# Kernel optimization log

Measured on AMD Instinct MI355X. Metric: run time of the kernel, lower is better.

Reference implementation:

```python
import jax, jax.numpy as jnp
import numpy as np

B, S, DIN, D, H = 32, 2048, 1024, 512, 8
NC, NM = 19, 10


def _mha(q_in, kv, Wq, bq, Wk, bk, Wv, bv, Wo, bo, add_mask):
    # q_in: [B,S,D]; kv: [K,D] (shared across batch); add_mask: [B,S,K] additive logit bias
    Bq, Sq, Dm = q_in.shape
    dh = Dm // H
    q = (q_in @ Wq + bq).reshape(Bq, Sq, H, dh)
    k = (kv @ Wk + bk).reshape(-1, H, dh)
    v = (kv @ Wv + bv).reshape(-1, H, dh)
    logits = jnp.einsum('bshd,khd->bhsk', q, k) / jnp.sqrt(jnp.float32(dh))
    attn = jax.nn.softmax(logits + add_mask[:, None, :, :], axis=-1)  # [B,H,S,K]
    out = jnp.einsum('bhsk,khd->bshd', attn, v).reshape(Bq, Sq, Dm)
    return out @ Wo + bo


def setup_inputs() -> dict:
    key = jax.random.key(0)
    ks = jax.random.split(key, 32)
    s = 0.02
    p = lambda i, shape: jax.random.normal(ks[i], shape, jnp.float32) * s
    z = lambda: jnp.zeros((D,), jnp.float32)
    return {
        'embeddings': jax.random.normal(ks[0], (B, S, DIN), jnp.float32),
        'embeddings_mask': jax.random.randint(ks[1], (B, S), 0, 2, jnp.int32),
        'post_mask': jax.random.randint(ks[2], (B, S), 0, 2, jnp.int32),
        'frame_mask': jax.random.randint(ks[3], (B, S), 0, 2, jnp.int32),
        'cultural_mask': jax.random.randint(ks[4], (B, NC), 0, 2, jnp.int32),
        'moral_mask': jax.random.randint(ks[5], (B, NM), 0, 2, jnp.int32),
        'W_lin': p(6, (DIN, D)), 'b_lin': z(),
        'cultural_table': p(7, (NC, D)), 'moral_table': p(8, (NM, D)),
        'c_Wq': p(9, (D, D)), 'c_bq': z(), 'c_Wk': p(10, (D, D)), 'c_bk': z(),
        'c_Wv': p(11, (D, D)), 'c_bv': z(), 'c_Wo': p(12, (D, D)), 'c_bo': z(),
        'm_Wq': p(13, (D, D)), 'm_bq': z(), 'm_Wk': p(14, (D, D)), 'm_bk': z(),
        'm_Wv': p(15, (D, D)), 'm_bv': z(), 'm_Wo': p(16, (D, D)), 'm_bo': z(),
    }


def reference(embeddings, embeddings_mask, post_mask, frame_mask, cultural_mask, moral_mask,
              W_lin, b_lin, cultural_table, moral_table,
              c_Wq, c_bq, c_Wk, c_bk, c_Wv, c_bv, c_Wo, c_bo,
              m_Wq, m_bq, m_Wk, m_bk, m_Wv, m_bv, m_Wo, m_bo):
    x = embeddings @ W_lin + b_lin  # [B,S,D]
    em = embeddings_mask.astype(jnp.float32)
    pm = em * post_mask.astype(jnp.float32)   # combined post mask [B,S]
    fm = em * frame_mask.astype(jnp.float32)  # combined frame mask [B,S]
    cm = cultural_mask.astype(jnp.float32)    # [B,NC]
    mm = moral_mask.astype(jnp.float32)       # [B,NM]
    cw = (c_Wq, c_bq, c_Wk, c_bk, c_Wv, c_bv, c_Wo, c_bo)
    mw = (m_Wq, m_bq, m_Wk, m_bk, m_Wv, m_bv, m_Wo, m_bo)
    # cultural branch: two stacked cross-attentions, float masks are ADDED to logits
    fc = _mha(x, cultural_table, *cw, fm[:, :, None] + cm[:, None, :])
    pc = _mha(fc, cultural_table, *cw, pm[:, :, None] + cm[:, None, :])
    post_cultural = pc.sum(axis=1) / pm.sum(axis=1, keepdims=True)
    # moral branch
    fmo = _mha(x, moral_table, *mw, fm[:, :, None] + mm[:, None, :])
    pmo = _mha(fmo, moral_table, *mw, pm[:, :, None] + mm[:, None, :])
    post_moral = pmo.sum(axis=1) / pm.sum(axis=1, keepdims=True)
    pooled = post_cultural - post_moral
    return post_cultural, pooled
```

## Files before the change

kernel.cpp:

```cpp
#include <hip/hip_runtime.h>
#include <math.h>

typedef __bf16 bf16;
typedef __bf16 bf16x8 __attribute__((ext_vector_type(8)));
typedef float floatx4 __attribute__((ext_vector_type(4)));

#define S_LEN 2048
#define BATCH 32
#define NHEAD 8
#define KC 19
#define KM 10
#define HKC 152
#define HKM 80
#define NTOT 232
#define NPAD 256
#define ROWS 64


__global__ __launch_bounds__(256) void prep1(
    const int* __restrict__ em, const int* __restrict__ pmask,
    const int* __restrict__ cmask, const int* __restrict__ mmask,
    const float* __restrict__ ctab, const float* __restrict__ mtab,
    const float* __restrict__ cWk, const float* __restrict__ cbk,
    const float* __restrict__ cWv, const float* __restrict__ cbv,
    const float* __restrict__ mWk, const float* __restrict__ mbk,
    const float* __restrict__ mWv, const float* __restrict__ mbv,
    float* __restrict__ P, float* __restrict__ A2, float* __restrict__ mb,
    float* __restrict__ k1c, float* __restrict__ v1c,
    float* __restrict__ k1m, float* __restrict__ v1m,
    bf16* __restrict__ GT, bf16* __restrict__ Bt,
    float* __restrict__ c1, float* __restrict__ c2)
{
    __shared__ float smem[512];
    const int blk = blockIdx.x, tid = threadIdx.x;

    if (blk < 32) {
        int* red = (int*)smem;
        int b = blk;
        int s = 0;
        for (int i = tid; i < S_LEN; i += 256) s += em[b*S_LEN+i] * pmask[b*S_LEN+i];
        red[tid] = s; __syncthreads();
        for (int o = 128; o; o >>= 1) { if (tid < o) red[tid] += red[tid+o]; __syncthreads(); }
        if (tid == 0) P[b] = (float)red[0];
        float v = 0.f;
        if (tid < HKC) v = (float)cmask[b*KC + (tid % KC)];
        else if (tid < NTOT) v = (float)mmask[b*KM + ((tid - HKC) % KM)];
        mb[b*NPAD + tid] = v;
        A2[b*NPAD + tid] = 0.f;
    } else if (blk < 61) {
        int r = blk - 32;
        const float* T;  const float* Wk; const float* bk; const float* Wv; const float* bv;
        float* k1; float* v1; int row;
        if (r < KC) { T = ctab; Wk = cWk; bk = cbk; Wv = cWv; bv = cbv; k1 = k1c; v1 = v1c; row = r; }
        else        { T = mtab; Wk = mWk; bk = mbk; Wv = mWv; bv = mbv; k1 = k1m; v1 = v1m; row = r - KC; }
        for (int i = tid; i < 512; i += 256) smem[i] = T[row*512+i];
        __syncthreads();
        for (int j = tid; j < 512; j += 256) {
            float sk = bk[j], sv = bv[j];
            for (int d = 0; d < 512; d++) { float t = smem[d]; sk += t*Wk[d*512+j]; sv += t*Wv[d*512+j]; }
            k1[row*512+j] = sk; v1[row*512+j] = sv;
        }
    } else {
        int z = blk - 61;
        for (int i = tid; i < 16384; i += 256) GT[z*16384 + i] = (bf16)0.f;
        for (int i = tid; i < 6144; i += 256) {
            int t = z*4 + (i / 1536);
            int j = i % 1536;
            Bt[(size_t)(t*256 + NTOT)*64 + j] = (bf16)0.f;
        }
        if (z == 0) { c1[tid] = 0.f; c2[tid] = 0.f; }
    }
}

__global__ __launch_bounds__(256) void prep2(
    const float* __restrict__ cWq, const float* __restrict__ mWq,
    const float* __restrict__ k1c, const float* __restrict__ v1c,
    const float* __restrict__ k1m, const float* __restrict__ v1m,
    const float* __restrict__ cWo, const float* __restrict__ mWo,
    float* __restrict__ MqTd, float* __restrict__ W2)
{
    __shared__ float smem[15872];
    const int blk = blockIdx.x, tid = threadIdx.x;

    if (blk < 512) {
        int D = blk;
        for (int i = tid; i < 9728; i += 256) smem[i] = k1c[i];
        for (int i = tid; i < 5120; i += 256) smem[9728+i] = k1m[i];
        for (int i = tid; i < 512; i += 256) {
            smem[14848+i] = cWq[(size_t)D*512+i];
            smem[15360+i] = mWq[(size_t)D*512+i];
        }
        __syncthreads();
        if (tid < HKC) {
            int h = tid / KC, k = tid % KC;
            const float* kr = smem + k*512 + h*64;
            float mq = 0.f;
            #pragma unroll 16
            for (int d = 0; d < 64; d++) mq += smem[14848 + h*64 + d] * kr[d];
            MqTd[D*NPAD + tid] = mq;
        }
        if (tid < HKM) {
            int h = tid / KM, k = tid % KM;
            const float* kr = smem + 9728 + k*512 + h*64;
            float mq = 0.f;
            #pragma unroll 16
            for (int d = 0; d < 64; d++) mq += smem[15360 + h*64 + d] * kr[d];
            MqTd[D*NPAD + HKC + tid] = mq;
        }
    } else {
        int n = blk - 512;
        const float* v1; const float* Wo; int h, k;
        if (n < HKC) { v1 = v1c; Wo = cWo; h = n / KC; k = n % KC; }
        else         { v1 = v1m; Wo = mWo; h = (n-HKC) / KM; k = (n-HKC) % KM; }
        if (tid < 64) smem[tid] = v1[k*512 + h*64 + tid];
        __syncthreads();
        for (int j = tid; j < 512; j += 256) {
            float s = 0.f;
            #pragma unroll 16
            for (int d = 0; d < 64; d++) s += smem[d] * Wo[(size_t)(h*64+d)*512 + j];
            W2[(size_t)n*512 + j] = s;
        }
    }
}

__global__ __launch_bounds__(256) void prep3(
    const float* __restrict__ W_lin, const float* __restrict__ b_lin,
    const float* __restrict__ MqTd, const float* __restrict__ W2,
    const float* __restrict__ k1c, const float* __restrict__ k1m,
    const float* __restrict__ cbq, const float* __restrict__ mbq,
    const float* __restrict__ cbo, const float* __restrict__ mbo,
    bf16* __restrict__ Bt, bf16* __restrict__ GT, float* __restrict__ c1, float* __restrict__ c2)
{
    __shared__ float smem[4096];
    const int blk = blockIdx.x, tid = threadIdx.x;

    if (blk < NTOT) {
        int n = blk;
        for (int i = tid; i < 512; i += 256) smem[i] = W2[(size_t)n*512 + i];
        __syncthreads();
        if (n < HKC) {
            for (int np = tid; np < HKC; np += 256) {
                float s = 0.f;
                for (int t = 0; t < 512; t++) s += smem[t] * MqTd[t*NPAD + np];
                GT[(size_t)np*NPAD + n] = (bf16)(0.125f*s);
            }
        } else {
            for (int np = tid; np < HKM; np += 256) {
                float s = 0.f;
                for (int t = 0; t < 512; t++) s += smem[t] * MqTd[t*NPAD + HKC + np];
                GT[(size_t)(HKC+np)*NPAD + n] = (bf16)(0.125f*s);
            }
        }
    } else if (blk < 360) {
        int D0 = (blk - NTOT) * 8;
        for (int i = tid; i < 4096; i += 256)
            smem[i] = W_lin[(size_t)(D0 + (i >> 9))*512 + (i & 511)];
        __syncthreads();
        if (tid < NTOT) {
            float acc[8] = {};
            for (int d = 0; d < 512; d++) {
                float m = MqTd[d*NPAD + tid];
                #pragma unroll
                for (int r = 0; r < 8; r++) acc[r] += smem[r*512 + d] * m;
            }
            int step = D0 >> 6, off = D0 & 63;
            #pragma unroll
            for (int r = 0; r < 8; r++)
                Bt[(size_t)(step*256 + tid)*64 + off + r] = (bf16)(0.125f*acc[r]);
        }
    } else {
        for (int i = tid; i < 512; i += 256) {
            smem[i] = b_lin[i];
            smem[512+i] = cbo[i];
            smem[1024+i] = mbo[i];
        }
        __syncthreads();
        if (tid < NTOT) {
            bool cult = tid < HKC;
            const float* bo_s = cult ? (smem+512) : (smem+1024);
            float sA = 0.f, sB = 0.f;
            for (int D = 0; D < 512; D++) {
                float m = MqTd[D*NPAD + tid];
                sA += smem[D]*m;
                sB += bo_s[D]*m;
            }
            float skq = 0.f;
            if (cult) {
                int h = tid / KC, k = tid % KC;
                for (int d = 0; d < 64; d++) skq += cbq[h*64+d] * k1c[k*512 + h*64 + d];
            } else {
                int nm = tid - HKC, h = nm / KM, k = nm % KM;
                for (int d = 0; d < 64; d++) skq += mbq[h*64+d] * k1m[k*512 + h*64 + d];
            }
            c1[tid] = 0.125f*(sA + skq);
            c2[tid] = 0.125f*(sB + skq);
        }
    }
}

__global__ __launch_bounds__(256, 3) void g12_kernel(const float* __restrict__ emb,
                                                     const bf16* __restrict__ Bt,
                                                     const bf16* __restrict__ GT,
                                                     const float* __restrict__ c1,
                                                     const float* __restrict__ c2,
                                                     const float* __restrict__ mb,
                                                     float* __restrict__ A2)
{
    __shared__ union UU {
        struct { bf16 As[ROWS*72]; bf16 Bs[256*72]; } s;
        bf16 Ls[ROWS*264];
    } u;
    __shared__ float bias1[256], bias2[256];
    const int tid = threadIdx.x;
    const int m0 = blockIdx.x*ROWS, b = blockIdx.x >> 5;
    bias1[tid] = c1[tid] + mb[b*NPAD + tid];
    bias2[tid] = c2[tid] + mb[b*NPAD + tid];
    const int wave = tid >> 6, lane = tid & 63, lr = lane & 15, kg = lane >> 4;
    floatx4 acc[4][4] = {};
    const int arow = tid >> 2, acol = (tid & 3)*16;
    const float* ap = emb + (size_t)(m0 + arow)*1024 + acol;
    bf16* asw = u.s.As + arow*72 + acol;
    const bf16* bp = Bt + (size_t)wave*4096 + lane*8;
    bf16* bsw = u.s.Bs + (size_t)(wave*64 + (lane >> 3))*72 + (lane & 7)*8;
    const bf16* afp = u.s.As + lr*72 + kg*8;
    const bf16* bfp = u.s.Bs + (wave*64 + lr)*72 + kg*8;

    float4 f0, f1, f2, f3;
    uint4 q0, q1, q2, q3, q4, q5, q6, q7;
    f0 = *(const float4*)(ap);      f1 = *(const float4*)(ap + 4);
    f2 = *(const float4*)(ap + 8);  f3 = *(const float4*)(ap + 12);
    q0 = *(const uint4*)(bp);        q1 = *(const uint4*)(bp + 512);
    q2 = *(const uint4*)(bp + 1024); q3 = *(const uint4*)(bp + 1536);
    q4 = *(const uint4*)(bp + 2048); q5 = *(const uint4*)(bp + 2560);
    q6 = *(const uint4*)(bp + 3072); q7 = *(const uint4*)(bp + 3584);
    #pragma unroll 1
    for (int t = 0; t < 16; t++) {
        asm volatile("s_waitcnt lgkmcnt(0)" ::: "memory");
        __builtin_amdgcn_s_barrier();
        {
            bf16x8 p0, p1;
            p0[0]=(bf16)f0.x; p0[1]=(bf16)f0.y; p0[2]=(bf16)f0.z; p0[3]=(bf16)f0.w;
            p0[4]=(bf16)f1.x; p0[5]=(bf16)f1.y; p0[6]=(bf16)f1.z; p0[7]=(bf16)f1.w;
            p1[0]=(bf16)f2.x; p1[1]=(bf16)f2.y; p1[2]=(bf16)f2.z; p1[3]=(bf16)f2.w;
            p1[4]=(bf16)f3.x; p1[5]=(bf16)f3.y; p1[6]=(bf16)f3.z; p1[7]=(bf16)f3.w;
            *(bf16x8*)asw = p0; *(bf16x8*)(asw + 8) = p1;
            *(uint4*)bsw = q0;          *(uint4*)(bsw + 576)  = q1;
            *(uint4*)(bsw + 1152) = q2; *(uint4*)(bsw + 1728) = q3;
            *(uint4*)(bsw + 2304) = q4; *(uint4*)(bsw + 2880) = q5;
            *(uint4*)(bsw + 3456) = q6; *(uint4*)(bsw + 4032) = q7;
        }
        if (t < 15) {
            const float* a2 = ap + (t + 1)*64;
            const bf16*  b2 = bp + (t + 1)*16384;
            f0 = *(const float4*)(a2);      f1 = *(const float4*)(a2 + 4);
            f2 = *(const float4*)(a2 + 8);  f3 = *(const float4*)(a2 + 12);
            q0 = *(const uint4*)(b2);        q1 = *(const uint4*)(b2 + 512);
            q2 = *(const uint4*)(b2 + 1024); q3 = *(const uint4*)(b2 + 1536);
            q4 = *(const uint4*)(b2 + 2048); q5 = *(const uint4*)(b2 + 2560);
            q6 = *(const uint4*)(b2 + 3072); q7 = *(const uint4*)(b2 + 3584);
        }
        asm volatile("s_waitcnt lgkmcnt(0)" ::: "memory");
        __builtin_amdgcn_s_barrier();
        #pragma unroll
        for (int kk = 0; kk < 64; kk += 32) {
            bf16x8 af[4], bfr[4];
            #pragma unroll
            for (int mi = 0; mi < 4; mi++) af[mi] = *(const bf16x8*)(afp + mi*16*72 + kk);
            #pragma unroll
            for (int nt = 0; nt < 4; nt++) bfr[nt] = *(const bf16x8*)(bfp + nt*16*72 + kk);
            #pragma unroll
            for (int mi = 0; mi < 4; mi++)
                #pragma unroll
                for (int nt = 0; nt < 4; nt++)
                    acc[mi][nt] = __builtin_amdgcn_mfma_f32_16x16x32_bf16(af[mi], bfr[nt], acc[mi][nt], 0, 0, 0);
        }
    }
    __syncthreads();
    #pragma unroll
    for (int nt = 0; nt < 4; nt++) {
        int col = wave*64 + nt*16 + lr;
        float bb = bias1[col];
        #pragma unroll
        for (int mi = 0; mi < 4; mi++) {
            int row = mi*16 + kg*4;
            #pragma unroll
            for (int r = 0; r < 4; r++)
                u.Ls[(row + r)*264 + col] = (bf16)(acc[mi][nt][r] + bb);
        }
    }
    __syncthreads();
    {
        int row = tid & 63, part = tid >> 6;
        bf16* Lr = u.Ls + row*264;
        if (part < 2) {
            for (int h = part*4; h < part*4 + 4; h++) {
                float lv[KC]; float m = -1e30f;
                #pragma unroll
                for (int j = 0; j < KC; j++) { lv[j] = (float)Lr[h*KC + j]; m = fmaxf(m, lv[j]); }
                float s = 0.f;
                #pragma unroll
                for (int j = 0; j < KC; j++) { lv[j] = __expf(lv[j] - m); s += lv[j]; }
                float inv = 1.f / s;
                #pragma unroll
                for (int j = 0; j < KC; j++) Lr[h*KC + j] = (bf16)(lv[j]*inv);
            }
        } else {
            for (int h = (part-2)*4; h < (part-2)*4 + 4; h++) {
                float lv[KM]; float m = -1e30f;
                #pragma unroll
                for (int j = 0; j < KM; j++) { lv[j] = (float)Lr[HKC + h*KM + j]; m = fmaxf(m, lv[j]); }
                float s = 0.f;
                #pragma unroll
                for (int j = 0; j < KM; j++) { lv[j] = __expf(lv[j] - m); s += lv[j]; }
                float inv = 1.f / s;
                #pragma unroll
                for (int j = 0; j < KM; j++) Lr[HKC + h*KM + j] = (bf16)(lv[j]*inv);
            }
            if (part == 3) for (int c = NTOT; c < NPAD; c++) Lr[c] = (bf16)0.f;
        }
    }
    __syncthreads();

    floatx4 acc2[4][4] = {};
    {
        const bf16* afp3 = u.Ls + lr*264 + kg*8;
        const bf16* gt0 = GT + (size_t)(wave*64 + lr)*NPAD + kg*8;
        #pragma unroll 2
        for (int t = 0; t < 8; t++) {
            bf16x8 gbv[4], af3[4];
            #pragma unroll
            for (int nt = 0; nt < 4; nt++) gbv[nt] = *(const bf16x8*)(gt0 + nt*16*NPAD + t*32);
            #pragma unroll
            for (int mi = 0; mi < 4; mi++) af3[mi] = *(const bf16x8*)(afp3 + mi*16*264 + t*32);
            #pragma unroll
            for (int mi = 0; mi < 4; mi++)
                #pragma unroll
                for (int nt = 0; nt < 4; nt++)
                    acc2[mi][nt] = __builtin_amdgcn_mfma_f32_16x16x32_bf16(af3[mi], gbv[nt], acc2[mi][nt], 0, 0, 0);
        }
    }
    __syncthreads();

    #pragma unroll
    for (int nt = 0; nt < 4; nt++) {
        int col = wave*64 + nt*16 + lr;
        float bb = bias2[col];
        #pragma unroll
        for (int mi = 0; mi < 4; mi++) {
            int row = mi*16 + kg*4;
            #pragma unroll
            for (int r = 0; r < 4; r++)
                u.Ls[(row + r)*264 + col] = (bf16)(acc2[mi][nt][r] + bb);
        }
    }
    __syncthreads();
    {
        int row = tid & 63, part = tid >> 6;
        bf16* Lr = u.Ls + row*264;
        if (part < 2) {
            for (int h = part*4; h < part*4 + 4; h++) {
                float lv[KC]; float m = -1e30f;
                #pragma unroll
                for (int j = 0; j < KC; j++) { lv[j] = (float)Lr[h*KC + j]; m = fmaxf(m, lv[j]); }
                float s = 0.f;
                #pragma unroll
                for (int j = 0; j < KC; j++) { lv[j] = __expf(lv[j] - m); s += lv[j]; }
                float inv = 1.f / s;
                #pragma unroll
                for (int j = 0; j < KC; j++) Lr[h*KC + j] = (bf16)(lv[j]*inv);
            }
        } else {
            for (int h = (part-2)*4; h < (part-2)*4 + 4; h++) {
                float lv[KM]; float m = -1e30f;
                #pragma unroll
                for (int j = 0; j < KM; j++) { lv[j] = (float)Lr[HKC + h*KM + j]; m = fmaxf(m, lv[j]); }
                float s = 0.f;
                #pragma unroll
                for (int j = 0; j < KM; j++) { lv[j] = __expf(lv[j] - m); s += lv[j]; }
                float inv = 1.f / s;
                #pragma unroll
                for (int j = 0; j < KM; j++) Lr[HKC + h*KM + j] = (bf16)(lv[j]*inv);
            }
        }
    }
    __syncthreads();
    {
        float s = 0.f;
        for (int r = 0; r < ROWS; r++) s += (float)u.Ls[r*264 + tid];
        if (tid < NTOT) atomicAdd(&A2[b*NPAD + tid], s);
    }
}

__global__ __launch_bounds__(256) void finalize_kernel(const float* __restrict__ A2, const float* __restrict__ W2,
                                                       const float* __restrict__ cbo, const float* __restrict__ mbo,
                                                       const float* __restrict__ P, float* __restrict__ out)
{
    __shared__ float a[NTOT];
    int b = blockIdx.x, tid = threadIdx.x;
    if (tid < NTOT) a[tid] = A2[b*NPAD + tid];
    __syncthreads();
    float invP = 1.f / P[b];
    for (int j = tid; j < 512; j += 256) {
        float pc = 2048.f*cbo[j], pm = 2048.f*mbo[j];
        for (int n = 0; n < HKC; n++) pc += a[n]*W2[n*512 + j];
        for (int n = HKC; n < NTOT; n++) pm += a[n]*W2[n*512 + j];
        out[b*512 + j] = pc*invP;
        out[BATCH*512 + b*512 + j] = (pc - pm)*invP;
    }
}

extern "C" void kernel_launch(void* const* d_in, const int* in_sizes, int n_in,
                              void* d_out, int out_size, void* d_ws, size_t ws_size,
                              hipStream_t stream)
{
    (void)in_sizes; (void)n_in; (void)out_size;
    const float* emb   = (const float*)d_in[0];
    const int* emask   = (const int*)d_in[1];
    const int* pmask   = (const int*)d_in[2];
    const int* cmask   = (const int*)d_in[4];
    const int* mmask   = (const int*)d_in[5];
    const float* W_lin = (const float*)d_in[6];
    const float* b_lin = (const float*)d_in[7];
    const float* ctab  = (const float*)d_in[8];
    const float* mtab  = (const float*)d_in[9];
    const float* cWq = (const float*)d_in[10]; const float* cbq = (const float*)d_in[11];
    const float* cWk = (const float*)d_in[12]; const float* cbk = (const float*)d_in[13];
    const float* cWv = (const float*)d_in[14]; const float* cbv = (const float*)d_in[15];
    const float* cWo = (const float*)d_in[16]; const float* cbo = (const float*)d_in[17];
    const float* mWq = (const float*)d_in[18]; const float* mbq = (const float*)d_in[19];
    const float* mWk = (const float*)d_in[20]; const float* mbk = (const float*)d_in[21];
    const float* mWv = (const float*)d_in[22]; const float* mbv = (const float*)d_in[23];
    const float* mWo = (const float*)d_in[24]; const float* mbo = (const float*)d_in[25];
    float* outp = (float*)d_out;

    if (ws_size < 40000000UL) return;

    char* ws = (char*)d_ws;
    size_t o = 0;
    bf16* Bt    = (bf16*)(ws + o); o += 256*1024*2;
    bf16* GT    = (bf16*)(ws + o); o += NPAD*NPAD*2;
    float* k1c  = (float*)(ws + o); o += KC*512*4;
    float* v1c  = (float*)(ws + o); o += KC*512*4;
    float* k1m  = (float*)(ws + o); o += KM*512*4;
    float* v1m  = (float*)(ws + o); o += KM*512*4;
    float* MqTd = (float*)(ws + o); o += (size_t)512*NPAD*4;
    float* W2   = (float*)(ws + o); o += (size_t)NTOT*512*4;
    float* c1   = (float*)(ws + o); o += NPAD*4;
    float* c2   = (float*)(ws + o); o += NPAD*4;
    float* mbt  = (float*)(ws + o); o += BATCH*NPAD*4;
    float* P    = (float*)(ws + o); o += 128;
    float* A2   = (float*)(ws + o); o += BATCH*NPAD*4;

    dim3 blk(256);

    prep1<<<dim3(65), blk, 0, stream>>>(emask, pmask, cmask, mmask, ctab, mtab,
                                        cWk, cbk, cWv, cbv, mWk, mbk, mWv, mbv,
                                        P, A2, mbt, k1c, v1c, k1m, v1m, GT, Bt, c1, c2);
    prep2<<<dim3(744), blk, 0, stream>>>(cWq, mWq, k1c, v1c, k1m, v1m, cWo, mWo, MqTd, W2);
    prep3<<<dim3(361), blk, 0, stream>>>(W_lin, b_lin, MqTd, W2, k1c, k1m,
                                         cbq, mbq, cbo, mbo, Bt, GT, c1, c2);
    g12_kernel<<<dim3(1024), blk, 0, stream>>>(emb, Bt, GT, c1, c2, mbt, A2);
    finalize_kernel<<<dim3(BATCH), blk, 0, stream>>>(A2, W2, cbo, mbo, P, outp);
}
```

Baseline: 602.9 us.

## Load B fragments directly to registers and double-buffer A tile in LDS

The GEMM main loop no longer stages the weight tile through shared memory. Each lane now loads its MFMA B fragments straight from global memory into registers, prefetched two iterations ahead. The A tile is double-buffered in LDS, so each iteration needs one barrier instead of two, and the LDS footprint shrinks. The cost is higher register pressure from 16 extra bf16x8 registers under launch_bounds(256,3), and B is read from global without cross-wave sharing.

```diff
diff --git a/kernel.cpp b/kernel.cpp
--- a/kernel.cpp
+++ b/kernel.cpp
@@ -207,7 +207,7 @@
                                                      float* __restrict__ A2)
 {
     __shared__ union UU {
-        struct { bf16 As[ROWS*72]; bf16 Bs[256*72]; } s;
+        bf16 As[2][ROWS*72];
         bf16 Ls[ROWS*264];
     } u;
     __shared__ float bias1[256], bias2[256];
@@ -219,61 +219,111 @@
     floatx4 acc[4][4] = {};
     const int arow = tid >> 2, acol = (tid & 3)*16;
     const float* ap = emb + (size_t)(m0 + arow)*1024 + acol;
-    bf16* asw = u.s.As + arow*72 + acol;
-    const bf16* bp = Bt + (size_t)wave*4096 + lane*8;
-    bf16* bsw = u.s.Bs + (size_t)(wave*64 + (lane >> 3))*72 + (lane & 7)*8;
-    const bf16* afp = u.s.As + lr*72 + kg*8;
-    const bf16* bfp = u.s.Bs + (wave*64 + lr)*72 + kg*8;
+    bf16* asw0 = u.As[0] + arow*72 + acol;
+    bf16* asw1 = u.As[1] + arow*72 + acol;
+    const bf16* afp0 = u.As[0] + lr*72 + kg*8;
+    const bf16* afp1 = u.As[1] + lr*72 + kg*8;
+    const bf16* bq = Bt + (size_t)((wave*64 + lr)*64 + kg*8);
 
     float4 f0, f1, f2, f3;
-    uint4 q0, q1, q2, q3, q4, q5, q6, q7;
+    bf16x8 b0,b1,b2,b3,b4,b5,b6,b7;
+    bf16x8 n0,n1,n2,n3,n4,n5,n6,n7;
     f0 = *(const float4*)(ap);      f1 = *(const float4*)(ap + 4);
     f2 = *(const float4*)(ap + 8);  f3 = *(const float4*)(ap + 12);
-    q0 = *(const uint4*)(bp);        q1 = *(const uint4*)(bp + 512);
-    q2 = *(const uint4*)(bp + 1024); q3 = *(const uint4*)(bp + 1536);
-    q4 = *(const uint4*)(bp + 2048); q5 = *(const uint4*)(bp + 2560);
-    q6 = *(const uint4*)(bp + 3072); q7 = *(const uint4*)(bp + 3584);
+    b0 = *(const bf16x8*)(bq);          b1 = *(const bf16x8*)(bq + 1024);
+    b2 = *(const bf16x8*)(bq + 2048);   b3 = *(const bf16x8*)(bq + 3072);
+    b4 = *(const bf16x8*)(bq + 32);     b5 = *(const bf16x8*)(bq + 1056);
+    b6 = *(const bf16x8*)(bq + 2080);   b7 = *(const bf16x8*)(bq + 3104);
+    {
+        bf16x8 p0, p1;
+        p0[0]=(bf16)f0.x; p0[1]=(bf16)f0.y; p0[2]=(bf16)f0.z; p0[3]=(bf16)f0.w;
+        p0[4]=(bf16)f1.x; p0[5]=(bf16)f1.y; p0[6]=(bf16)f1.z; p0[7]=(bf16)f1.w;
+        p1[0]=(bf16)f2.x; p1[1]=(bf16)f2.y; p1[2]=(bf16)f2.z; p1[3]=(bf16)f2.w;
+        p1[4]=(bf16)f3.x; p1[5]=(bf16)f3.y; p1[6]=(bf16)f3.z; p1[7]=(bf16)f3.w;
+        *(bf16x8*)asw0 = p0; *(bf16x8*)(asw0 + 8) = p1;
+    }
+    f0 = *(const float4*)(ap + 64);  f1 = *(const float4*)(ap + 68);
+    f2 = *(const float4*)(ap + 72);  f3 = *(const float4*)(ap + 76);
+    n0 = *(const bf16x8*)(bq + 16384);        n1 = *(const bf16x8*)(bq + 17408);
+    n2 = *(const bf16x8*)(bq + 18432);        n3 = *(const bf16x8*)(bq + 19456);
+    n4 = *(const bf16x8*)(bq + 16416);        n5 = *(const bf16x8*)(bq + 17440);
+    n6 = *(const bf16x8*)(bq + 18464);        n7 = *(const bf16x8*)(bq + 19488);
+    asm volatile("s_waitcnt lgkmcnt(0)" ::: "memory");
+    __builtin_amdgcn_s_barrier();
+
+    bf16* wptr = asw1; bf16* walt = asw0;
+    const bf16* rptr = afp0; const bf16* ralt = afp1;
     #pragma unroll 1
     for (int t = 0; t < 16; t++) {
-        asm volatile("s_waitcnt lgkmcnt(0)" ::: "memory");
-        __builtin_amdgcn_s_barrier();
-        {
+        if (t < 15) {
             bf16x8 p0, p1;
             p0[0]=(bf16)f0.x; p0[1]=(bf16)f0.y; p0[2]=(bf16)f0.z; p0[3]=(bf16)f0.w;
             p0[4]=(bf16)f1.x; p0[5]=(bf16)f1.y; p0[6]=(bf16)f1.z; p0[7]=(bf16)f1.w;
             p1[0]=(bf16)f2.x; p1[1]=(bf16)f2.y; p1[2]=(bf16)f2.z; p1[3]=(bf16)f2.w;
             p1[4]=(bf16)f3.x; p1[5]=(bf16)f3.y; p1[6]=(bf16)f3.z; p1[7]=(bf16)f3.w;
-            *(bf16x8*)asw = p0; *(bf16x8*)(asw + 8) = p1;
-            *(uint4*)bsw = q0;          *(uint4*)(bsw + 576)  = q1;
-            *(uint4*)(bsw + 1152) = q2; *(uint4*)(bsw + 1728) = q3;
-            *(uint4*)(bsw + 2304) = q4; *(uint4*)(bsw + 2880) = q5;
-            *(uint4*)(bsw + 3456) = q6; *(uint4*)(bsw + 4032) = q7;
-        }
-        if (t < 15) {
-            const float* a2 = ap + (t + 1)*64;
-            const bf16*  b2 = bp + (t + 1)*16384;
+            *(bf16x8*)wptr = p0; *(bf16x8*)(wptr + 8) = p1;
+        }
+        if (t < 14) {
+            const float* a2 = ap + (t + 2)*64;
             f0 = *(const float4*)(a2);      f1 = *(const float4*)(a2 + 4);
             f2 = *(const float4*)(a2 + 8);  f3 = *(const float4*)(a2 + 12);
-            q0 = *(const uint4*)(b2);        q1 = *(const uint4*)(b2 + 512);
-            q2 = *(const uint4*)(b2 + 1024); q3 = *(const uint4*)(b2 + 1536);
-            q4 = *(const uint4*)(b2 + 2048); q5 = *(const uint4*)(b2 + 2560);
-            q6 = *(const uint4*)(b2 + 3072); q7 = *(const uint4*)(b2 + 3584);
-        }
+        }
+        {
+            bf16x8 a0 = *(const bf16x8*)(rptr);
+            bf16x8 a1 = *(const bf16x8*)(rptr + 1152);
+            bf16x8 a2v = *(const bf16x8*)(rptr + 2304);
+            bf16x8 a3 = *(const bf16x8*)(rptr + 3456);
+            acc[0][0] = __builtin_amdgcn_mfma_f32_16x16x32_bf16(a0, b0, acc[0][0], 0, 0, 0);
+            acc[0][1] = __builtin_amdgcn_mfma_f32_16x16x32_bf16(a0, b1, acc[0][1], 0, 0, 0);
+            acc[0][2] = __builtin_amdgcn_mfma_f32_16x16x32_bf16(a0, b2, acc[0][2], 0, 0, 0);
+            acc[0][3] = __builtin_amdgcn_mfma_f32_16x16x32_bf16(a0, b3, acc[0][3], 0, 0, 0);
+            acc[1][0] = __builtin_amdgcn_mfma_f32_16x16x32_bf16(a1, b0, acc[1][0], 0, 0, 0);
+            acc[1][1] = __builtin_amdgcn_mfma_f32_16x16x32_bf16(a1, b1, acc[1][1], 0, 0, 0);
+            acc[1][2] = __builtin_amdgcn_mfma_f32_16x16x32_bf16(a1, b2, acc[1][2], 0, 0, 0);
+            acc[1][3] = __builtin_amdgcn_mfma_f32_16x16x32_bf16(a1, b3, acc[1][3], 0, 0, 0);
+            acc[2][0] = __builtin_amdgcn_mfma_f32_16x16x32_bf16(a2v, b0, acc[2][0], 0, 0, 0);
+            acc[2][1] = __builtin_amdgcn_mfma_f32_16x16x32_bf16(a2v, b1, acc[2][1], 0, 0, 0);
+            acc[2][2] = __builtin_amdgcn_mfma_f32_16x16x32_bf16(a2v, b2, acc[2][2], 0, 0, 0);
+            acc[2][3] = __builtin_amdgcn_mfma_f32_16x16x32_bf16(a2v, b3, acc[2][3], 0, 0, 0);
+            acc[3][0] = __builtin_amdgcn_mfma_f32_16x16x32_bf16(a3, b0, acc[3][0], 0, 0, 0);
+            acc[3][1] = __builtin_amdgcn_mfma_f32_16x16x32_bf16(a3, b1, acc[3][1], 0, 0, 0);
+            acc[3][2] = __builtin_amdgcn_mfma_f32_16x16x32_bf16(a3, b2, acc[3][2], 0, 0, 0);
+            acc[3][3] = __builtin_amdgcn_mfma_f32_16x16x32_bf16(a3, b3, acc[3][3], 0, 0, 0);
+            a0 = *(const bf16x8*)(rptr + 32);
+            a1 = *(const bf16x8*)(rptr + 1184);
+            a2v = *(const bf16x8*)(rptr + 2336);
+            a3 = *(const bf16x8*)(rptr + 3488);
+            acc[0][0] = __builtin_amdgcn_mfma_f32_16x16x32_bf16(a0, b4, acc[0][0], 0, 0, 0);
+            acc[0][1] = __builtin_amdgcn_mfma_f32_16x16x32_bf16(a0, b5, acc[0][1], 0, 0, 0);
+            acc[0][2] = __builtin_amdgcn_mfma_f32_16x16x32_bf16(a0, b6, acc[0][2], 0, 0, 0);
+            acc[0][3] = __builtin_amdgcn_mfma_f32_16x16x32_bf16(a0, b7, acc[0][3], 0, 0, 0);
+            acc[1][0] = __builtin_amdgcn_mfma_f32_16x16x32_bf16(a1, b4, acc[1][0], 0, 0, 0);
+            acc[1][1] = __builtin_amdgcn_mfma_f32_16x16x32_bf16(a1, b5, acc[1][1], 0, 0, 0);
+            acc[1][2] = __builtin_amdgcn_mfma_f32_16x16x32_bf16(a1, b6, acc[1][2], 0, 0, 0);
+            acc[1][3] = __builtin_amdgcn_mfma_f32_16x16x32_bf16(a1, b7, acc[1][3], 0, 0, 0);
+            acc[2][0] = __builtin_amdgcn_mfma_f32_16x16x32_bf16(a2v, b4, acc[2][0], 0, 0, 0);
+            acc[2][1] = __builtin_amdgcn_mfma_f32_16x16x32_bf16(a2v, b5, acc[2][1], 0, 0, 0);
+            acc[2][2] = __builtin_amdgcn_mfma_f32_16x16x32_bf16(a2v, b6, acc[2][2], 0, 0, 0);
+            acc[2][3] = __builtin_amdgcn_mfma_f32_16x16x32_bf16(a2v, b7, acc[2][3], 0, 0, 0);
+            acc[3][0] = __builtin_amdgcn_mfma_f32_16x16x32_bf16(a3, b4, acc[3][0], 0, 0, 0);
+            acc[3][1] = __builtin_amdgcn_mfma_f32_16x16x32_bf16(a3, b5, acc[3][1], 0, 0, 0);
+            acc[3][2] = __builtin_amdgcn_mfma_f32_16x16x32_bf16(a3, b6, acc[3][2], 0, 0, 0);
+            acc[3][3] = __builtin_amdgcn_mfma_f32_16x16x32_bf16(a3, b7, acc[3][3], 0, 0, 0);
+        }
+        if (t < 15) {
+            b0 = n0; b1 = n1; b2 = n2; b3 = n3; b4 = n4; b5 = n5; b6 = n6; b7 = n7;
+        }
+        if (t < 14) {
+            const bf16* b2p = bq + (size_t)(t + 2)*16384;
+            n0 = *(const bf16x8*)(b2p);         n1 = *(const bf16x8*)(b2p + 1024);
+            n2 = *(const bf16x8*)(b2p + 2048);  n3 = *(const bf16x8*)(b2p + 3072);
+            n4 = *(const bf16x8*)(b2p + 32);    n5 = *(const bf16x8*)(b2p + 1056);
+            n6 = *(const bf16x8*)(b2p + 2080);  n7 = *(const bf16x8*)(b2p + 3104);
+        }
+        { bf16* tw = wptr; wptr = walt; walt = tw; }
+        { const bf16* tr = rptr; rptr = ralt; ralt = tr; }
         asm volatile("s_waitcnt lgkmcnt(0)" ::: "memory");
         __builtin_amdgcn_s_barrier();
-        #pragma unroll
-        for (int kk = 0; kk < 64; kk += 32) {
-            bf16x8 af[4], bfr[4];
-            #pragma unroll
-            for (int mi = 0; mi < 4; mi++) af[mi] = *(const bf16x8*)(afp + mi*16*72 + kk);
-            #pragma unroll
-            for (int nt = 0; nt < 4; nt++) bfr[nt] = *(const bf16x8*)(bfp + nt*16*72 + kk);
-            #pragma unroll
-            for (int mi = 0; mi < 4; mi++)
-                #pragma unroll
-                for (int nt = 0; nt < 4; nt++)
-                    acc[mi][nt] = __builtin_amdgcn_mfma_f32_16x16x32_bf16(af[mi], bfr[nt], acc[mi][nt], 0, 0, 0);
-        }
     }
     __syncthreads();
     #pragma unroll
```

Result: slower. 619.5 us (+2.8%).
